# Performance work log

Measured on AMD Instinct MI355X. Metric: run time of the kernel, lower is better.

The kernel has to match this reference:

```python
import jax, jax.numpy as jnp
import numpy as np

EPS = 1e-4  # softmax_kernel eps

def softmax_kernel(data, projection, is_query):
    # data: [b,h,n,d], projection: [m,d]
    d = data.shape[-1]
    m = projection.shape[0]
    data_normalizer = d ** -0.25
    ratio = m ** -0.5
    data_dash = jnp.einsum('bhnd,md->bhnm', data_normalizer * data, projection)
    diag_data = (jnp.sum(data ** 2, axis=-1) * 0.5 * data_normalizer ** 2)[..., None]  # [b,h,n,1]
    if is_query:
        stab = jnp.max(data_dash, axis=-1, keepdims=True)
    else:
        stab = jnp.max(data_dash)
    return ratio * (jnp.exp(data_dash - diag_data - stab) + EPS)

def linear_attention(q, k, v):
    # q,k: [b,h,n,m]; v: [b,h,n,e]
    k_cumsum = jnp.sum(k, axis=-2)                                  # [b,h,m]
    D_inv = 1.0 / jnp.einsum('bhnm,bhm->bhn', q, k_cumsum)          # [b,h,n]
    context = jnp.einsum('bhnm,bhne->bhme', k, v)                   # [b,h,m,e]
    return jnp.einsum('bhme,bhnm,bhn->bhne', context, q, D_inv)     # [b,h,n,e]

def setup_inputs() -> dict:
    key = jax.random.key(0)
    kq, kk, kv, kp = jax.random.split(key, 4)
    B, H, N, D = 4, 8, 4096, 64
    M = 266  # int(64 * ln(64))
    q = jax.random.normal(kq, (B, H, N, D), dtype=jnp.float32)
    k = jax.random.normal(kk, (B, H, N, D), dtype=jnp.float32)
    v = jax.random.normal(kv, (B, H, N, D), dtype=jnp.float32)
    # Gaussian random-feature projection (stand-in for orthogonal blocks; same math path)
    projection = jax.random.normal(kp, (M, D), dtype=jnp.float32)
    return {"q": q, "k": k, "v": v, "projection": projection}

def reference(q, k, v, projection):
    q_prime = softmax_kernel(q, projection, is_query=True)
    k_prime = softmax_kernel(k, projection, is_query=False)
    return linear_attention(q_prime, k_prime, v)
```

## Files before the change

### kernel.cpp

```cpp
#include <hip/hip_runtime.h>
#include <math.h>

#define NN 4096
#define DD 64
#define MM 266
#define MP 272
#define NORMZ 0.35355339059327379f
#define RATIO 0.06131393394849658f
#define EPSV 1e-4f
#define NEG_INF (-3.4e38f)
#define LSTR 72
#define GSTR 320

typedef __attribute__((ext_vector_type(8))) short bfrag;
typedef __attribute__((ext_vector_type(4))) float f32x4;

#define MFMA(a, b, c) __builtin_amdgcn_mfma_f32_16x16x32_bf16((a), (b), (c), 0, 0, 0)

__device__ inline ushort bf16rne(float x) {
    union { float f; unsigned u; } c; c.f = x;
    unsigned r = c.u + 0x7FFFu + ((c.u >> 16) & 1u);
    return (ushort)(r >> 16);
}
__device__ inline float bf2f(ushort h) {
    union { unsigned u; float f; } c; c.u = ((unsigned)h) << 16;
    return c.f;
}
__device__ inline void splitf(float x, ushort& h, ushort& l) {
    h = bf16rne(x);
    l = bf16rne(x - bf2f(h));
}
__device__ inline void pack8(const float4& a, const float4& b, bfrag& H, bfrag& L) {
    ushort h, l;
    splitf(a.x, h, l); H[0] = (short)h; L[0] = (short)l;
    splitf(a.y, h, l); H[1] = (short)h; L[1] = (short)l;
    splitf(a.z, h, l); H[2] = (short)h; L[2] = (short)l;
    splitf(a.w, h, l); H[3] = (short)h; L[3] = (short)l;
    splitf(b.x, h, l); H[4] = (short)h; L[4] = (short)l;
    splitf(b.y, h, l); H[5] = (short)h; L[5] = (short)l;
    splitf(b.z, h, l); H[6] = (short)h; L[6] = (short)l;
    splitf(b.w, h, l); H[7] = (short)h; L[7] = (short)l;
}

__global__ void proj_split(const float* __restrict__ proj,
                           ushort* __restrict__ pH, ushort* __restrict__ pL)
{
    int i = (blockIdx.x * 256 + threadIdx.x) * 4;
    int m = i >> 6;
    float4 x = (m < MM) ? *(const float4*)(proj + i) : make_float4(0.f, 0.f, 0.f, 0.f);
    ushort h0, l0, h1, l1, h2, l2, h3, l3;
    splitf(x.x, h0, l0); splitf(x.y, h1, l1); splitf(x.z, h2, l2); splitf(x.w, h3, l3);
    *(ushort4*)(pH + i) = make_ushort4(h0, h1, h2, h3);
    *(ushort4*)(pL + i) = make_ushort4(l0, l1, l2, l3);
}

__launch_bounds__(256, 2)
__global__ void kpass(const float* __restrict__ kin, const float* __restrict__ vin,
                      const ushort* __restrict__ pjH, const ushort* __restrict__ pjL,
                      float* __restrict__ ctxP, float* __restrict__ kcP,
                      float* __restrict__ pmax, float* __restrict__ vsum)
{
    __shared__ ushort dataH[64 * LSTR], dataLo[64 * LSTR];
    __shared__ ushort vTH[64 * LSTR], vTLo[64 * LSTR];
    __shared__ ushort r2H[64 * LSTR], r2Lo[64 * LSTR];
    __shared__ float kcS[MP];
    __shared__ float redS[4];
    __shared__ float vredS[DD];

    const int t = threadIdx.x;
    const int w = t >> 6;
    const int lane = t & 63;
    const int l15 = lane & 15;
    const int q = lane >> 4;
    const int hd = blockIdx.y;
    const int nb = blockIdx.x;

    kcS[t] = 0.f;
    if (t < 16) kcS[256 + t] = 0.f;
    if (t < DD) vredS[t] = 0.f;

    const f32x4 zf = {0.f, 0.f, 0.f, 0.f};
    f32x4 cacc[4][4];
    f32x4 cacc4 = zf;
    #pragma unroll
    for (int c = 0; c < 4; ++c)
        #pragma unroll
        for (int e = 0; e < 4; ++e) cacc[c][e] = zf;
    float bmaxl = NEG_INF;
    float4 vacc = make_float4(0.f, 0.f, 0.f, 0.f);

    #pragma unroll 1
    for (int st = 0; st < 4; ++st) {
        const int n0 = (nb << 8) + (st << 6);
        __syncthreads();

        const float* vb = vin + ((size_t)hd * NN + n0) * DD;
        #pragma unroll
        for (int j = 0; j < 4; ++j) {
            int i = (t + (j << 8)) << 2;
            int n = i >> 6, e = i & 63;
            float4 x = *(const float4*)(vb + i);
            vacc.x += x.x; vacc.y += x.y; vacc.z += x.z; vacc.w += x.w;
            ushort h, l;
            splitf(x.x, h, l); vTH[(e + 0) * LSTR + n] = h; vTLo[(e + 0) * LSTR + n] = l;
            splitf(x.y, h, l); vTH[(e + 1) * LSTR + n] = h; vTLo[(e + 1) * LSTR + n] = l;
            splitf(x.z, h, l); vTH[(e + 2) * LSTR + n] = h; vTLo[(e + 2) * LSTR + n] = l;
            splitf(x.w, h, l); vTH[(e + 3) * LSTR + n] = h; vTLo[(e + 3) * LSTR + n] = l;
        }

        const float* kb = kin + ((size_t)hd * NN + n0) * DD;
        const int row = (w << 4) + l15;
        float4 x0 = *(const float4*)(kb + (row << 6) + (q << 3));
        float4 x1 = *(const float4*)(kb + (row << 6) + (q << 3) + 4);
        float4 x2 = *(const float4*)(kb + (row << 6) + 32 + (q << 3));
        float4 x3 = *(const float4*)(kb + (row << 6) + 32 + (q << 3) + 4);
        x0.x *= NORMZ; x0.y *= NORMZ; x0.z *= NORMZ; x0.w *= NORMZ;
        x1.x *= NORMZ; x1.y *= NORMZ; x1.z *= NORMZ; x1.w *= NORMZ;
        x2.x *= NORMZ; x2.y *= NORMZ; x2.z *= NORMZ; x2.w *= NORMZ;
        x3.x *= NORMZ; x3.y *= NORMZ; x3.z *= NORMZ; x3.w *= NORMZ;
        float ss = x0.x*x0.x + x0.y*x0.y + x0.z*x0.z + x0.w*x0.w
                 + x1.x*x1.x + x1.y*x1.y + x1.z*x1.z + x1.w*x1.w
                 + x2.x*x2.x + x2.y*x2.y + x2.z*x2.z + x2.w*x2.w
                 + x3.x*x3.x + x3.y*x3.y + x3.z*x3.z + x3.w*x3.w;
        ss += __shfl_xor(ss, 16);
        ss += __shfl_xor(ss, 32);
        float dg[4];
        #pragma unroll
        for (int r = 0; r < 4; ++r) dg[r] = 0.5f * __shfl(ss, (q << 2) + r);
        bfrag aH[2], aL[2];
        pack8(x0, x1, aH[0], aL[0]);
        pack8(x2, x3, aH[1], aL[1]);
        __syncthreads();

        #pragma unroll
        for (int c = 0; c < 5; ++c) {
            const int mtiles = (c < 4) ? 4 : 1;
            const int m0 = c << 6;
            {
                const int tot = mtiles << 7;
                for (int idx = t; idx < tot; idx += 256) {
                    int i = idx << 3; int r = i >> 6, cc = i & 63;
                    *(uint4*)&r2H[r * LSTR + cc] = *(const uint4*)(pjH + ((m0 + r) << 6) + cc);
                    *(uint4*)&r2Lo[r * LSTR + cc] = *(const uint4*)(pjL + ((m0 + r) << 6) + cc);
                }
            }
            __syncthreads();

            f32x4 dd4[4];
            #pragma unroll
            for (int mt = 0; mt < 4; ++mt) {
                if (mt >= mtiles) break;
                const int mrow = (mt << 4) + l15;
                bfrag bH0 = *(const bfrag*)&r2H[mrow * LSTR + (q << 3)];
                bfrag bH1 = *(const bfrag*)&r2H[mrow * LSTR + 32 + (q << 3)];
                bfrag bL0 = *(const bfrag*)&r2Lo[mrow * LSTR + (q << 3)];
                bfrag bL1 = *(const bfrag*)&r2Lo[mrow * LSTR + 32 + (q << 3)];
                f32x4 a = zf;
                a = MFMA(aH[0], bL0, a);
                a = MFMA(aH[1], bL1, a);
                a = MFMA(aL[0], bH0, a);
                a = MFMA(aL[1], bH1, a);
                a = MFMA(aH[0], bH0, a);
                a = MFMA(aH[1], bH1, a);
                dd4[mt] = a;
            }
            #pragma unroll
            for (int mt = 0; mt < 4; ++mt) {
                if (mt >= mtiles) break;
                const int mg = m0 + (mt << 4) + l15;
                const bool valid = (mg < MM);
                ushort uh[4], ul[4];
                float csum = 0.f;
                #pragma unroll
                for (int reg = 0; reg < 4; ++reg) {
                    float dv = dd4[mt][reg];
                    float u = 0.f;
                    if (valid) {
                        bmaxl = fmaxf(bmaxl, dv);
                        u = __expf(dv - dg[reg]);
                    }
                    csum += u;
                    splitf(u, uh[reg], ul[reg]);
                }
                *(ushort4*)&dataH[((mt << 4) + l15) * LSTR + (w << 4) + (q << 2)] =
                    make_ushort4(uh[0], uh[1], uh[2], uh[3]);
                *(ushort4*)&dataLo[((mt << 4) + l15) * LSTR + (w << 4) + (q << 2)] =
                    make_ushort4(ul[0], ul[1], ul[2], ul[3]);
                csum += __shfl_xor(csum, 16);
                csum += __shfl_xor(csum, 32);
                if (q == 0) atomicAdd(&kcS[mg], csum);
            }
            __syncthreads();

            if (c < 4) {
                const int mrow = (w << 4) + l15;
                bfrag uH0 = *(const bfrag*)&dataH[mrow * LSTR + (q << 3)];
                bfrag uH1 = *(const bfrag*)&dataH[mrow * LSTR + 32 + (q << 3)];
                bfrag uL0 = *(const bfrag*)&dataLo[mrow * LSTR + (q << 3)];
                bfrag uL1 = *(const bfrag*)&dataLo[mrow * LSTR + 32 + (q << 3)];
                #pragma unroll
                for (int et = 0; et < 4; ++et) {
                    const int erow = (et << 4) + l15;
                    bfrag vH0 = *(const bfrag*)&vTH[erow * LSTR + (q << 3)];
                    bfrag vH1 = *(const bfrag*)&vTH[erow * LSTR + 32 + (q << 3)];
                    bfrag vL0 = *(const bfrag*)&vTLo[erow * LSTR + (q << 3)];
                    bfrag vL1 = *(const bfrag*)&vTLo[erow * LSTR + 32 + (q << 3)];
                    f32x4 a = cacc[c][et];
                    a = MFMA(uH0, vL0, a);
                    a = MFMA(uH1, vL1, a);
                    a = MFMA(uL0, vH0, a);
                    a = MFMA(uL1, vH1, a);
                    a = MFMA(uH0, vH0, a);
                    a = MFMA(uH1, vH1, a);
                    cacc[c][et] = a;
                }
            } else {
                const int mrow = l15;
                bfrag uH0 = *(const bfrag*)&dataH[mrow * LSTR + (q << 3)];
                bfrag uH1 = *(const bfrag*)&dataH[mrow * LSTR + 32 + (q << 3)];
                bfrag uL0 = *(const bfrag*)&dataLo[mrow * LSTR + (q << 3)];
                bfrag uL1 = *(const bfrag*)&dataLo[mrow * LSTR + 32 + (q << 3)];
                const int erow = (w << 4) + l15;
                bfrag vH0 = *(const bfrag*)&vTH[erow * LSTR + (q << 3)];
                bfrag vH1 = *(const bfrag*)&vTH[erow * LSTR + 32 + (q << 3)];
                bfrag vL0 = *(const bfrag*)&vTLo[erow * LSTR + (q << 3)];
                bfrag vL1 = *(const bfrag*)&vTLo[erow * LSTR + 32 + (q << 3)];
                f32x4 a = cacc4;
                a = MFMA(uH0, vL0, a);
                a = MFMA(uH1, vL1, a);
                a = MFMA(uL0, vH0, a);
                a = MFMA(uL1, vH1, a);
                a = MFMA(uH0, vH0, a);
                a = MFMA(uH1, vH1, a);
                cacc4 = a;
            }
        }
    }

    __syncthreads();
    {
        float bm = bmaxl;
        #pragma unroll
        for (int d = 1; d < 64; d <<= 1) bm = fmaxf(bm, __shfl_xor(bm, d));
        if (lane == 0) redS[w] = bm;
    }
    {
        const int e0 = (t << 2) & 63;
        atomicAdd(&vredS[e0 + 0], vacc.x);
        atomicAdd(&vredS[e0 + 1], vacc.y);
        atomicAdd(&vredS[e0 + 2], vacc.z);
        atomicAdd(&vredS[e0 + 3], vacc.w);
    }
    __syncthreads();
    if (t == 0) pmax[hd * 16 + nb] = fmaxf(fmaxf(redS[0], redS[1]), fmaxf(redS[2], redS[3]));
    if (t < DD) atomicAdd(&vsum[hd * DD + t], vredS[t]);
    for (int m = t; m < MP; m += 256) kcP[(size_t)(hd * 16 + nb) * MP + m] = kcS[m];
    float* cp = ctxP + (size_t)(hd * 16 + nb) * MP * DD;
    #pragma unroll
    for (int c = 0; c < 4; ++c) {
        const int mbase = (c << 6) + (w << 4) + (q << 2);
        #pragma unroll
        for (int et = 0; et < 4; ++et)
            #pragma unroll
            for (int reg = 0; reg < 4; ++reg)
                cp[(mbase + reg) * DD + (et << 4) + l15] = cacc[c][et][reg];
    }
    #pragma unroll
    for (int reg = 0; reg < 4; ++reg)
        cp[(256 + (q << 2) + reg) * DD + (w << 4) + l15] = cacc4[reg];
}

__global__ void ctx_reduce(const float* __restrict__ ctxP, const float* __restrict__ kcP,
                           const float* __restrict__ vsum, const float* __restrict__ pmax,
                           ushort* __restrict__ gH, ushort* __restrict__ gL,
                           float* __restrict__ kcF)
{
    __shared__ ushort hiT[64][20], loT[64][20];
    __shared__ float rmxS[4];
    const int t = threadIdx.x, mt = blockIdx.x, hd = blockIdx.y;
    const int lane = t & 63, w = t >> 6;
    float mxl = fmaxf(pmax[t], pmax[t + 256]);
    #pragma unroll
    for (int d = 1; d < 64; d <<= 1) mxl = fmaxf(mxl, __shfl_xor(mxl, d));
    if (lane == 0) rmxS[w] = mxl;
    __syncthreads();
    const float stab = fmaxf(fmaxf(rmxS[0], rmxS[1]), fmaxf(rmxS[2], rmxS[3]));
    const float Asc = RATIO * __expf(-stab);
    const float REPS = RATIO * EPSV;
    const int e = t & 63, mq = t >> 6;
    const float vs = vsum[hd * DD + e];
    #pragma unroll
    for (int i = 0; i < 4; ++i) {
        const int ml = mq * 4 + i;
        const int m = mt * 16 + ml;
        float s = 0.f;
        for (int nbk = 0; nbk < 16; ++nbk)
            s += ctxP[((size_t)(hd * 16 + nbk) * MP + m) * DD + e];
        float val = Asc * s + REPS * vs;
        ushort h, l; splitf(val, h, l);
        hiT[e][ml] = h; loT[e][ml] = l;
    }
    __syncthreads();
    {
        const int i = t * 4, e2 = i >> 4, cc = i & 15;
        ushort4 hv = make_ushort4(hiT[e2][cc], hiT[e2][cc + 1], hiT[e2][cc + 2], hiT[e2][cc + 3]);
        ushort4 lv = make_ushort4(loT[e2][cc], loT[e2][cc + 1], loT[e2][cc + 2], loT[e2][cc + 3]);
        *(ushort4*)(gH + ((size_t)hd * 64 + e2) * GSTR + mt * 16 + cc) = hv;
        *(ushort4*)(gL + ((size_t)hd * 64 + e2) * GSTR + mt * 16 + cc) = lv;
    }
    if (t < 16) {
        const int m = mt * 16 + t;
        float s = 0.f;
        for (int nbk = 0; nbk < 16; ++nbk) s += kcP[(size_t)(hd * 16 + nbk) * MP + m];
        kcF[hd * MP + m] = Asc * s + ((m < MM) ? REPS * (float)NN : 0.f);
    }
}

__launch_bounds__(256, 4)
__global__ void qpass(const float* __restrict__ qin,
                      const ushort* __restrict__ pjH, const ushort* __restrict__ pjL,
                      const ushort* __restrict__ gH, const ushort* __restrict__ gL,
                      const float* __restrict__ kcF,
                      float* __restrict__ outp)
{
    __shared__ ushort bPH[64 * LSTR], bPL[64 * LSTR];
    __shared__ ushort bQH[64 * LSTR], bQL[64 * LSTR];

    const int t = threadIdx.x;
    const int w = t >> 6;
    const int lane = t & 63;
    const int l15 = lane & 15;
    const int q = lane >> 4;
    const int hd = blockIdx.y;
    const int n0 = blockIdx.x << 6;

    const float* qb = qin + ((size_t)hd * NN + n0) * DD;
    const int row = (w << 4) + l15;
    float4 x0 = *(const float4*)(qb + (row << 6) + (q << 3));
    float4 x1 = *(const float4*)(qb + (row << 6) + (q << 3) + 4);
    float4 x2 = *(const float4*)(qb + (row << 6) + 32 + (q << 3));
    float4 x3 = *(const float4*)(qb + (row << 6) + 32 + (q << 3) + 4);
    x0.x *= NORMZ; x0.y *= NORMZ; x0.z *= NORMZ; x0.w *= NORMZ;
    x1.x *= NORMZ; x1.y *= NORMZ; x1.z *= NORMZ; x1.w *= NORMZ;
    x2.x *= NORMZ; x2.y *= NORMZ; x2.z *= NORMZ; x2.w *= NORMZ;
    x3.x *= NORMZ; x3.y *= NORMZ; x3.z *= NORMZ; x3.w *= NORMZ;
    float ss = x0.x*x0.x + x0.y*x0.y + x0.z*x0.z + x0.w*x0.w
             + x1.x*x1.x + x1.y*x1.y + x1.z*x1.z + x1.w*x1.w
             + x2.x*x2.x + x2.y*x2.y + x2.z*x2.z + x2.w*x2.w
             + x3.x*x3.x + x3.y*x3.y + x3.z*x3.z + x3.w*x3.w;
    ss += __shfl_xor(ss, 16);
    ss += __shfl_xor(ss, 32);
    float dg[4];
    #pragma unroll
    for (int r = 0; r < 4; ++r) dg[r] = 0.5f * __shfl(ss, (q << 2) + r);
    bfrag aH[2], aL[2];
    pack8(x0, x1, aH[0], aL[0]);
    pack8(x2, x3, aH[1], aL[1]);

    const f32x4 zf = {0.f, 0.f, 0.f, 0.f};
    f32x4 ddq[17];

    #pragma unroll
    for (int c = 0; c < 5; ++c) {
        const int mtiles = (c < 4) ? 4 : 1;
        const int m0 = c << 6;
        __syncthreads();
        {
            const int tot = mtiles << 7;
            for (int idx = t; idx < tot; idx += 256) {
                int i = idx << 3; int r = i >> 6, cc = i & 63;
                *(uint4*)&bPH[r * LSTR + cc] = *(const uint4*)(pjH + ((m0 + r) << 6) + cc);
                *(uint4*)&bPL[r * LSTR + cc] = *(const uint4*)(pjL + ((m0 + r) << 6) + cc);
            }
        }
        __syncthreads();
        #pragma unroll
        for (int mt = 0; mt < 4; ++mt) {
            if (mt >= mtiles) break;
            const int mrow = (mt << 4) + l15;
            bfrag bH0 = *(const bfrag*)&bPH[mrow * LSTR + (q << 3)];
            bfrag bH1 = *(const bfrag*)&bPH[mrow * LSTR + 32 + (q << 3)];
            bfrag bL0 = *(const bfrag*)&bPL[mrow * LSTR + (q << 3)];
            bfrag bL1 = *(const bfrag*)&bPL[mrow * LSTR + 32 + (q << 3)];
            f32x4 a = zf;
            a = MFMA(aH[0], bL0, a);
            a = MFMA(aH[1], bL1, a);
            a = MFMA(aL[0], bH0, a);
            a = MFMA(aL[1], bH1, a);
            a = MFMA(aH[0], bH0, a);
            a = MFMA(aH[1], bH1, a);
            ddq[c * 4 + mt] = a;
        }
    }

    float rmax[4];
    #pragma unroll
    for (int reg = 0; reg < 4; ++reg) {
        float mx = NEG_INF;
        #pragma unroll
        for (int ti = 0; ti < 17; ++ti) {
            bool valid = (ti < 16) || (l15 < 10);
            if (valid) mx = fmaxf(mx, ddq[ti][reg]);
        }
        #pragma unroll
        for (int d = 1; d < 16; d <<= 1) mx = fmaxf(mx, __shfl_xor(mx, d));
        rmax[reg] = mx;
    }
    #pragma unroll
    for (int ti = 0; ti < 17; ++ti) {
        #pragma unroll
        for (int reg = 0; reg < 4; ++reg) {
            bool valid = (ti < 16) || (l15 < 10);
            float e = 0.f;
            if (valid)
                e = RATIO * (__expf(ddq[ti][reg] - dg[reg] - rmax[reg]) + EPSV);
            ddq[ti][reg] = e;
        }
    }
    float dinv[4];
    {
        const float* kcb = kcF + hd * MP;
        float den[4] = {0.f, 0.f, 0.f, 0.f};
        #pragma unroll
        for (int ti = 0; ti < 17; ++ti) {
            float kv = kcb[(ti << 4) + l15];
            #pragma unroll
            for (int reg = 0; reg < 4; ++reg) den[reg] += ddq[ti][reg] * kv;
        }
        #pragma unroll
        for (int reg = 0; reg < 4; ++reg) {
            #pragma unroll
            for (int d = 1; d < 16; d <<= 1) den[reg] += __shfl_xor(den[reg], d);
            dinv[reg] = 1.f / den[reg];
        }
    }

    f32x4 oacc[4];
    #pragma unroll
    for (int et = 0; et < 4; ++et) oacc[et] = zf;

    #pragma unroll
    for (int c = 0; c < 5; ++c) {
        const int mtiles = (c < 4) ? 4 : 1;
        __syncthreads();
        #pragma unroll
        for (int mt = 0; mt < 4; ++mt) {
            if (mt >= mtiles) break;
            const int ml = (mt << 4) + l15;
            #pragma unroll
            for (int reg = 0; reg < 4; ++reg) {
                ushort hh, ll; splitf(ddq[c * 4 + mt][reg], hh, ll);
                bPH[((w << 4) + (q << 2) + reg) * LSTR + ml] = hh;
                bPL[((w << 4) + (q << 2) + reg) * LSTR + ml] = ll;
            }
        }
        if (c == 4) {
            const int rown = (w << 4) + l15;
            *(ushort4*)&bPH[rown * LSTR + 16 + (q << 2)] = make_ushort4(0, 0, 0, 0);
            *(ushort4*)&bPL[rown * LSTR + 16 + (q << 2)] = make_ushort4(0, 0, 0, 0);
        }
        {
            for (int idx = t; idx < 512; idx += 256) {
                int i = idx << 3; int e = i >> 6, mm = i & 63;
                *(uint4*)&bQH[e * LSTR + mm] =
                    *(const uint4*)(gH + ((size_t)hd * 64 + e) * GSTR + (c << 6) + mm);
                *(uint4*)&bQL[e * LSTR + mm] =
                    *(const uint4*)(gL + ((size_t)hd * 64 + e) * GSTR + (c << 6) + mm);
            }
        }
        __syncthreads();
        const int arow = (w << 4) + l15;
        bfrag pH0 = *(const bfrag*)&bPH[arow * LSTR + (q << 3)];
        bfrag pL0 = *(const bfrag*)&bPL[arow * LSTR + (q << 3)];
        bfrag pH1, pL1;
        if (c < 4) {
            pH1 = *(const bfrag*)&bPH[arow * LSTR + 32 + (q << 3)];
            pL1 = *(const bfrag*)&bPL[arow * LSTR + 32 + (q << 3)];
        }
        #pragma unroll
        for (int et = 0; et < 4; ++et) {
            const int erow = (et << 4) + l15;
            bfrag cH0 = *(const bfrag*)&bQH[erow * LSTR + (q << 3)];
            bfrag cL0 = *(const bfrag*)&bQL[erow * LSTR + (q << 3)];
            f32x4 a = oacc[et];
            a = MFMA(pH0, cL0, a);
            a = MFMA(pL0, cH0, a);
            a = MFMA(pH0, cH0, a);
            if (c < 4) {
                bfrag cH1 = *(const bfrag*)&bQH[erow * LSTR + 32 + (q << 3)];
                bfrag cL1 = *(const bfrag*)&bQL[erow * LSTR + 32 + (q << 3)];
                a = MFMA(pH1, cL1, a);
                a = MFMA(pL1, cH1, a);
                a = MFMA(pH1, cH1, a);
            }
            oacc[et] = a;
        }
    }

    float* ob = outp + ((size_t)hd * NN + n0) * DD;
    #pragma unroll
    for (int et = 0; et < 4; ++et)
        #pragma unroll
        for (int reg = 0; reg < 4; ++reg)
            ob[((w << 4) + (q << 2) + reg) * DD + (et << 4) + l15] = oacc[et][reg] * dinv[reg];
}

extern "C" void kernel_launch(void* const* d_in, const int* in_sizes, int n_in,
                              void* d_out, int out_size, void* d_ws, size_t ws_size,
                              hipStream_t stream)
{
    const float* q = (const float*)d_in[0];
    const float* k = (const float*)d_in[1];
    const float* v = (const float*)d_in[2];
    const float* proj = (const float*)d_in[3];
    float* out = (float*)d_out;
    char* ws = (char*)d_ws;

    ushort* gH  = (ushort*)(ws);
    ushort* gL  = (ushort*)(ws + 1310720);
    float*  vsm = (float*)(ws + 2621440);
    ushort* pH  = (ushort*)(ws + 2629632);
    ushort* pL  = (ushort*)(ws + 2664448);
    float*  kcF = (float*)(ws + 2699264);
    float*  ctxP= (float*)(ws + 2734080);
    float*  kcP = (float*)(ws + 38385664);
    float*  pmax= (float*)(ws + 38942720);

    hipMemsetAsync(ws, 0, 2629632, stream);

    proj_split<<<dim3(17), 256, 0, stream>>>(proj, pH, pL);
    kpass<<<dim3(16, 32), 256, 0, stream>>>(k, v, pH, pL, ctxP, kcP, pmax, vsm);
    ctx_reduce<<<dim3(17, 32), 256, 0, stream>>>(ctxP, kcP, vsm, pmax, gH, gL, kcF);
    qpass<<<dim3(64, 32), 256, 0, stream>>>(q, pH, pL, gH, gL, kcF, out);
}
```

Baseline: 242.8 us.

## Reduce kpass partials with global atomics and transpose V via shuffles

The context and k-cumsum partials from the 16 n-blocks per head are now accumulated into one shared buffer with float atomicAdd. Previously each block wrote its own slice and ctx_reduce summed 16 slices, which removes the large partial-buffer round trip through memory. The V transpose into LDS now uses cross-lane shuffles so each lane writes packed ushort4 values instead of scattered 16-bit stores. The costs are atomic contention, a larger memset, and a nondeterministic summation order.

Result: slower. 250.9 us (+3.3%).

```diff
diff --git a/kernel.cpp b/kernel.cpp
--- a/kernel.cpp
+++ b/kernel.cpp
@@ -57,7 +57,7 @@
 __launch_bounds__(256, 2)
 __global__ void kpass(const float* __restrict__ kin, const float* __restrict__ vin,
                       const ushort* __restrict__ pjH, const ushort* __restrict__ pjL,
-                      float* __restrict__ ctxP, float* __restrict__ kcP,
+                      float* __restrict__ ctxA, float* __restrict__ kcA,
                       float* __restrict__ pmax, float* __restrict__ vsum)
 {
     __shared__ ushort dataH[64 * LSTR], dataLo[64 * LSTR];
@@ -98,14 +98,28 @@
         #pragma unroll
         for (int j = 0; j < 4; ++j) {
             int i = (t + (j << 8)) << 2;
-            int n = i >> 6, e = i & 63;
             float4 x = *(const float4*)(vb + i);
             vacc.x += x.x; vacc.y += x.y; vacc.z += x.z; vacc.w += x.w;
-            ushort h, l;
-            splitf(x.x, h, l); vTH[(e + 0) * LSTR + n] = h; vTLo[(e + 0) * LSTR + n] = l;
-            splitf(x.y, h, l); vTH[(e + 1) * LSTR + n] = h; vTLo[(e + 1) * LSTR + n] = l;
-            splitf(x.z, h, l); vTH[(e + 2) * LSTR + n] = h; vTLo[(e + 2) * LSTR + n] = l;
-            splitf(x.w, h, l); vTH[(e + 3) * LSTR + n] = h; vTLo[(e + 3) * LSTR + n] = l;
+            const bool qlo = (q < 2), qev = ((q & 1) == 0);
+            float r0 = __shfl_xor(qlo ? x.z : x.x, 32);
+            float r1 = __shfl_xor(qlo ? x.w : x.y, 32);
+            float z0 = qlo ? x.x : r0;
+            float z1 = qlo ? x.y : r1;
+            float z2 = qlo ? r0 : x.z;
+            float z3 = qlo ? r1 : x.w;
+            float s0 = __shfl_xor(qev ? z1 : z0, 16);
+            float s1 = __shfl_xor(qev ? z3 : z2, 16);
+            float T0 = qev ? z0 : s0;
+            float T1 = qev ? s0 : z1;
+            float T2 = qev ? z2 : s1;
+            float T3 = qev ? s1 : z3;
+            const int e = (l15 << 2) + q;
+            const int nb4 = (w << 2) + (j << 4);
+            ushort h0, l0, h1, l1, h2, l2, h3, l3;
+            splitf(T0, h0, l0); splitf(T1, h1, l1);
+            splitf(T2, h2, l2); splitf(T3, h3, l3);
+            *(ushort4*)&vTH[e * LSTR + nb4] = make_ushort4(h0, h1, h2, h3);
+            *(ushort4*)&vTLo[e * LSTR + nb4] = make_ushort4(l0, l1, l2, l3);
         }
 
         const float* kb = kin + ((size_t)hd * NN + n0) * DD;
@@ -254,8 +268,8 @@
     __syncthreads();
     if (t == 0) pmax[hd * 16 + nb] = fmaxf(fmaxf(redS[0], redS[1]), fmaxf(redS[2], redS[3]));
     if (t < DD) atomicAdd(&vsum[hd * DD + t], vredS[t]);
-    for (int m = t; m < MP; m += 256) kcP[(size_t)(hd * 16 + nb) * MP + m] = kcS[m];
-    float* cp = ctxP + (size_t)(hd * 16 + nb) * MP * DD;
+    for (int m = t; m < MP; m += 256) atomicAdd(&kcA[hd * MP + m], kcS[m]);
+    float* cp = ctxA + (size_t)hd * MP * DD;
     #pragma unroll
     for (int c = 0; c < 4; ++c) {
         const int mbase = (c << 6) + (w << 4) + (q << 2);
@@ -263,14 +277,14 @@
         for (int et = 0; et < 4; ++et)
             #pragma unroll
             for (int reg = 0; reg < 4; ++reg)
-                cp[(mbase + reg) * DD + (et << 4) + l15] = cacc[c][et][reg];
+                atomicAdd(&cp[(mbase + reg) * DD + (et << 4) + l15], cacc[c][et][reg]);
     }
     #pragma unroll
     for (int reg = 0; reg < 4; ++reg)
-        cp[(256 + (q << 2) + reg) * DD + (w << 4) + l15] = cacc4[reg];
-}
-
-__global__ void ctx_reduce(const float* __restrict__ ctxP, const float* __restrict__ kcP,
+        atomicAdd(&cp[(256 + (q << 2) + reg) * DD + (w << 4) + l15], cacc4[reg]);
+}
+
+__global__ void ctx_reduce(const float* __restrict__ ctxA, const float* __restrict__ kcA,
                            const float* __restrict__ vsum, const float* __restrict__ pmax,
                            ushort* __restrict__ gH, ushort* __restrict__ gL,
                            float* __restrict__ kcF)
@@ -293,9 +307,7 @@
     for (int i = 0; i < 4; ++i) {
         const int ml = mq * 4 + i;
         const int m = mt * 16 + ml;
-        float s = 0.f;
-        for (int nbk = 0; nbk < 16; ++nbk)
-            s += ctxP[((size_t)(hd * 16 + nbk) * MP + m) * DD + e];
+        float s = ctxA[((size_t)hd * MP + m) * DD + e];
         float val = Asc * s + REPS * vs;
         ushort h, l; splitf(val, h, l);
         hiT[e][ml] = h; loT[e][ml] = l;
@@ -310,9 +322,7 @@
     }
     if (t < 16) {
         const int m = mt * 16 + t;
-        float s = 0.f;
-        for (int nbk = 0; nbk < 16; ++nbk) s += kcP[(size_t)(hd * 16 + nbk) * MP + m];
-        kcF[hd * MP + m] = Asc * s + ((m < MM) ? REPS * (float)NN : 0.f);
+        kcF[hd * MP + m] = Asc * kcA[hd * MP + m] + ((m < MM) ? REPS * (float)NN : 0.f);
     }
 }
 
@@ -519,17 +529,17 @@
     ushort* gH  = (ushort*)(ws);
     ushort* gL  = (ushort*)(ws + 1310720);
     float*  vsm = (float*)(ws + 2621440);
-    ushort* pH  = (ushort*)(ws + 2629632);
-    ushort* pL  = (ushort*)(ws + 2664448);
-    float*  kcF = (float*)(ws + 2699264);
-    float*  ctxP= (float*)(ws + 2734080);
-    float*  kcP = (float*)(ws + 38385664);
-    float*  pmax= (float*)(ws + 38942720);
-
-    hipMemsetAsync(ws, 0, 2629632, stream);
+    float*  ctxA= (float*)(ws + 2629632);
+    float*  kcA = (float*)(ws + 4857856);
+    ushort* pH  = (ushort*)(ws + 4892672);
+    ushort* pL  = (ushort*)(ws + 4927488);
+    float*  kcF = (float*)(ws + 4962304);
+    float*  pmax= (float*)(ws + 4997120);
+
+    hipMemsetAsync(ws, 0, 4892672, stream);
 
     proj_split<<<dim3(17), 256, 0, stream>>>(proj, pH, pL);
-    kpass<<<dim3(16, 32), 256, 0, stream>>>(k, v, pH, pL, ctxP, kcP, pmax, vsm);
-    ctx_reduce<<<dim3(17, 32), 256, 0, stream>>>(ctxP, kcP, vsm, pmax, gH, gL, kcF);
+    kpass<<<dim3(16, 32), 256, 0, stream>>>(k, v, pH, pL, ctxA, kcA, pmax, vsm);
+    ctx_reduce<<<dim3(17, 32), 256, 0, stream>>>(ctxA, kcA, vsm, pmax, gH, gL, kcF);
     qpass<<<dim3(64, 32), 256, 0, stream>>>(q, pH, pL, gH, gL, kcF, out);
 }
```
